# Performance work log

Measured on AMD Instinct MI355X. Metric: run time of the kernel, lower is better.

The kernel has to match this reference:

```python
import jax, jax.numpy as jnp
import numpy as np

EMB = 1024
HEADS = 16
HEAD_DIM = EMB // HEADS


def setup_inputs() -> dict:
    key = jax.random.key(0)
    ks = jax.random.split(key, 5)
    x = jax.random.normal(ks[0], (2, 2048, EMB), dtype=jnp.float32)
    # per-head projection params, stacked over heads: [H, E, D]
    Wq = jax.random.normal(ks[1], (HEADS, EMB, HEAD_DIM), dtype=jnp.float32)
    Wk = jax.random.normal(ks[2], (HEADS, EMB, HEAD_DIM), dtype=jnp.float32)
    Wv = jax.random.normal(ks[3], (HEADS, EMB, HEAD_DIM), dtype=jnp.float32)
    # output projection (torch Linear weight [out, in], bias=False)
    Wo = jax.random.normal(ks[4], (EMB, EMB), dtype=jnp.float32) * (1.0 / np.sqrt(EMB))
    return {"x": x, "Wq": Wq, "Wk": Wk, "Wv": Wv, "Wo": Wo}


def reference(x, Wq, Wk, Wv, Wo):
    B, T, E = x.shape
    # per-head projections: [B, H, T, D]
    q = jnp.einsum('bte,hed->bhtd', x, Wq)
    k = jnp.einsum('bte,hed->bhtd', x, Wk)
    v = jnp.einsum('bte,hed->bhtd', x, Wv)
    scale = 1.0 / jnp.sqrt(jnp.asarray(HEAD_DIM, dtype=x.dtype))
    scores = jnp.einsum('bhtd,bhsd->bhts', q, k) * scale  # [B,H,T,T]
    s = jax.nn.softmax(scores, axis=-1)
    out = jnp.einsum('bhts,bhsd->bhtd', s, v)
    # concat heads along last dim in head order: [B, T, H*D]
    combined = jnp.transpose(out, (0, 2, 1, 3)).reshape(B, T, E)
    # residual + output projection (Linear bias=False: y = combined @ Wo.T)
    return x + combined @ Wo.T
```

## Files before the change

### kernel.cpp

```cpp
#include <hip/hip_runtime.h>

#define EMB   1024
#define HEADS 16
#define HDIM  64
#define BATCH 2
#define SEQ   2048
#define MROWS (BATCH*SEQ)
#define STR   40

typedef __attribute__((ext_vector_type(8))) short bf16x8;
typedef __attribute__((ext_vector_type(4))) float f32x4;
typedef unsigned short u16;

__device__ __forceinline__ u16 f2bf(float f) {
    unsigned u = __float_as_uint(f);
    u += 0x7fffu + ((u >> 16) & 1u);
    return (u16)(u >> 16);
}
__device__ __forceinline__ float bf2f(u16 h) {
    return __uint_as_float((unsigned)h << 16);
}

__global__ __launch_bounds__(256)
void xsplit(const float* __restrict__ X, u16* __restrict__ Xh,
            u16* __restrict__ Xl)
{
    int i = (blockIdx.x * 256 + threadIdx.x) * 8;
#pragma unroll
    for (int half = 0; half < 2; ++half) {
        float4 v = *(const float4*)(X + i + half * 4);
        ushort4 hi, lo;
        hi.x = f2bf(v.x); lo.x = f2bf(v.x - bf2f(hi.x));
        hi.y = f2bf(v.y); lo.y = f2bf(v.y - bf2f(hi.y));
        hi.z = f2bf(v.z); lo.z = f2bf(v.z - bf2f(hi.z));
        hi.w = f2bf(v.w); lo.w = f2bf(v.w - bf2f(hi.w));
        *(ushort4*)(Xh + i + half * 4) = hi;
        *(ushort4*)(Xl + i + half * 4) = lo;
    }
}

__global__ __launch_bounds__(256)
void wtrans(const float* __restrict__ Wq, const float* __restrict__ Wk,
            u16* __restrict__ Qth, u16* __restrict__ Qtl,
            u16* __restrict__ Kth, u16* __restrict__ Ktl)
{
    const float* W  = blockIdx.z ? Wk  : Wq;
    u16* Oh         = blockIdx.z ? Kth : Qth;
    u16* Ol         = blockIdx.z ? Ktl : Qtl;
    const int h  = blockIdx.y;
    const int d  = threadIdx.x & 63;
    const int e0 = (blockIdx.x * 4 + (threadIdx.x >> 6)) * 8;

    const float* src = W + ((size_t)h * EMB + e0) * HDIM + d;
    ushort4 h0, h1, l0, l1;
    float v; u16 hv;
    v = src[0 * 64]; hv = f2bf(v); h0.x = hv; l0.x = f2bf(v - bf2f(hv));
    v = src[1 * 64]; hv = f2bf(v); h0.y = hv; l0.y = f2bf(v - bf2f(hv));
    v = src[2 * 64]; hv = f2bf(v); h0.z = hv; l0.z = f2bf(v - bf2f(hv));
    v = src[3 * 64]; hv = f2bf(v); h0.w = hv; l0.w = f2bf(v - bf2f(hv));
    v = src[4 * 64]; hv = f2bf(v); h1.x = hv; l1.x = f2bf(v - bf2f(hv));
    v = src[5 * 64]; hv = f2bf(v); h1.y = hv; l1.y = f2bf(v - bf2f(hv));
    v = src[6 * 64]; hv = f2bf(v); h1.z = hv; l1.z = f2bf(v - bf2f(hv));
    v = src[7 * 64]; hv = f2bf(v); h1.w = hv; l1.w = f2bf(v - bf2f(hv));

    size_t obase = ((size_t)h * HDIM + d) * EMB + e0;
    *(ushort4*)(Oh + obase)     = h0;
    *(ushort4*)(Oh + obase + 4) = h1;
    *(ushort4*)(Ol + obase)     = l0;
    *(ushort4*)(Ol + obase + 4) = l1;
}

__global__ __launch_bounds__(256)
void wtrans_v(const float* __restrict__ Wv, u16* __restrict__ Vth)
{
    const int h  = blockIdx.y;
    const int d  = threadIdx.x & 63;
    const int e0 = (blockIdx.x * 4 + (threadIdx.x >> 6)) * 8;
    const float* src = Wv + ((size_t)h * EMB + e0) * HDIM + d;
    ushort4 h0, h1;
    h0.x = f2bf(src[0 * 64]); h0.y = f2bf(src[1 * 64]);
    h0.z = f2bf(src[2 * 64]); h0.w = f2bf(src[3 * 64]);
    h1.x = f2bf(src[4 * 64]); h1.y = f2bf(src[5 * 64]);
    h1.z = f2bf(src[6 * 64]); h1.w = f2bf(src[7 * 64]);
    size_t obase = ((size_t)h * HDIM + d) * EMB + e0;
    *(ushort4*)(Vth + obase)     = h0;
    *(ushort4*)(Vth + obase + 4) = h1;
}

__global__ __launch_bounds__(256)
void conv_bf16(const float* __restrict__ src, u16* __restrict__ dst)
{
    int i = (blockIdx.x * 256 + threadIdx.x) * 4;
    float4 v = *(const float4*)(src + i);
    ushort4 o;
    o.x = f2bf(v.x); o.y = f2bf(v.y); o.z = f2bf(v.z); o.w = f2bf(v.w);
    *(ushort4*)(dst + i) = o;
}

__global__ __launch_bounds__(256)
void qkv_z01(const u16* __restrict__ Xh, const u16* __restrict__ Xl,
             const u16* __restrict__ Wqh, const u16* __restrict__ Wql,
             const u16* __restrict__ Wkh, const u16* __restrict__ Wkl,
             u16* __restrict__ Qh, u16* __restrict__ Ql,
             u16* __restrict__ Kh, u16* __restrict__ Kl)
{
    const int z  = blockIdx.z;
    const int m0 = blockIdx.x * 128;
    const int n0 = blockIdx.y * 128;
    const int t    = threadIdx.x;
    const int wave = t >> 6, lane = t & 63;
    const int wm = wave & 1, wn = wave >> 1;
    const int l16 = lane & 15, quad = lane >> 4;

    __shared__ u16 Ahs[128][STR];
    __shared__ u16 Als[128][STR];
    __shared__ u16 Bhs[128][STR];
    __shared__ u16 Bls[128][STR];

    const u16* Bh_g = z ? Wkh : Wqh;
    const u16* Bl_g = z ? Wkl : Wql;

    const int ar0 = t >> 2, ak = (t & 3) * 8, ar1 = ar0 + 64;

    f32x4 acc[4][4];
#pragma unroll
    for (int i = 0; i < 4; ++i)
#pragma unroll
        for (int j = 0; j < 4; ++j) acc[i][j] = (f32x4){0.f, 0.f, 0.f, 0.f};

    bf16x8 cur[8], nxt[8];
#define QK_LOAD(dst, kk)                                                        \
    do {                                                                        \
        dst[0] = *(const bf16x8*)(Xh  + (size_t)(m0 + ar0) * EMB + (kk) + ak);  \
        dst[1] = *(const bf16x8*)(Xh  + (size_t)(m0 + ar1) * EMB + (kk) + ak);  \
        dst[2] = *(const bf16x8*)(Xl  + (size_t)(m0 + ar0) * EMB + (kk) + ak);  \
        dst[3] = *(const bf16x8*)(Xl  + (size_t)(m0 + ar1) * EMB + (kk) + ak);  \
        dst[4] = *(const bf16x8*)(Bh_g + (size_t)(n0 + ar0) * EMB + (kk) + ak); \
        dst[5] = *(const bf16x8*)(Bh_g + (size_t)(n0 + ar1) * EMB + (kk) + ak); \
        dst[6] = *(const bf16x8*)(Bl_g + (size_t)(n0 + ar0) * EMB + (kk) + ak); \
        dst[7] = *(const bf16x8*)(Bl_g + (size_t)(n0 + ar1) * EMB + (kk) + ak); \
    } while (0)

    QK_LOAD(cur, 0);

    for (int k0 = 0; k0 < EMB; k0 += 32) {
        __syncthreads();
        *(bf16x8*)&Ahs[ar0][ak] = cur[0];  *(bf16x8*)&Ahs[ar1][ak] = cur[1];
        *(bf16x8*)&Als[ar0][ak] = cur[2];  *(bf16x8*)&Als[ar1][ak] = cur[3];
        *(bf16x8*)&Bhs[ar0][ak] = cur[4];  *(bf16x8*)&Bhs[ar1][ak] = cur[5];
        *(bf16x8*)&Bls[ar0][ak] = cur[6];  *(bf16x8*)&Bls[ar1][ak] = cur[7];
        __syncthreads();

        const int kn = (k0 + 32 < EMB) ? k0 + 32 : 0;
        QK_LOAD(nxt, kn);

        bf16x8 B4h[4], B4l[4];
#pragma unroll
        for (int j = 0; j < 4; ++j) {
            B4h[j] = *(const bf16x8*)&Bhs[wn * 64 + 16 * j + l16][quad * 8];
            B4l[j] = *(const bf16x8*)&Bls[wn * 64 + 16 * j + l16][quad * 8];
        }
#pragma unroll
        for (int i = 0; i < 4; ++i) {
            bf16x8 Ai_h = *(const bf16x8*)&Ahs[wm * 64 + 16 * i + l16][quad * 8];
            bf16x8 Ai_l = *(const bf16x8*)&Als[wm * 64 + 16 * i + l16][quad * 8];
#pragma unroll
            for (int j = 0; j < 4; ++j) {
                acc[i][j] = __builtin_amdgcn_mfma_f32_16x16x32_bf16(Ai_h, B4h[j], acc[i][j], 0, 0, 0);
                acc[i][j] = __builtin_amdgcn_mfma_f32_16x16x32_bf16(Ai_h, B4l[j], acc[i][j], 0, 0, 0);
                acc[i][j] = __builtin_amdgcn_mfma_f32_16x16x32_bf16(Ai_l, B4h[j], acc[i][j], 0, 0, 0);
            }
        }
#pragma unroll
        for (int q = 0; q < 8; ++q) cur[q] = nxt[q];
    }
#undef QK_LOAD

    const int b = m0 >> 11;
    const int h = (n0 + wn * 64) >> 6;
    u16* Oh = z ? Kh : Qh;
    u16* Ol = z ? Kl : Ql;
#pragma unroll
    for (int i = 0; i < 4; ++i)
#pragma unroll
        for (int r = 0; r < 4; ++r) {
            int tt = (m0 & (SEQ - 1)) + wm * 64 + 16 * i + quad * 4 + r;
            size_t rowbase = ((size_t)(b * HEADS + h) * SEQ + tt) * HDIM;
#pragma unroll
            for (int j = 0; j < 4; ++j) {
                int d = 16 * j + l16;
                float v = acc[i][j][r];
                u16 hv = f2bf(v);
                Oh[rowbase + d] = hv;
                Ol[rowbase + d] = f2bf(v - bf2f(hv));
            }
        }
}

__global__ __launch_bounds__(256)
void qkv_v(const u16* __restrict__ Xh, const u16* __restrict__ Wvt,
           u16* __restrict__ Vt)
{
    const int m0 = blockIdx.x * 128;
    const int n0 = blockIdx.y * 128;
    const int t    = threadIdx.x;
    const int wave = t >> 6, lane = t & 63;
    const int wm = wave & 1, wn = wave >> 1;
    const int l16 = lane & 15, quad = lane >> 4;

    __shared__ u16 Ahs[128][STR];
    __shared__ u16 Bhs[128][STR];

    const int ar0 = t >> 2, ak = (t & 3) * 8, ar1 = ar0 + 64;

    f32x4 acc[4][4];
#pragma unroll
    for (int i = 0; i < 4; ++i)
#pragma unroll
        for (int j = 0; j < 4; ++j) acc[i][j] = (f32x4){0.f, 0.f, 0.f, 0.f};

    bf16x8 cur[4], nxt[4];
#define V_LOAD(dst, kk)                                                         \
    do {                                                                        \
        dst[0] = *(const bf16x8*)(Xh  + (size_t)(m0 + ar0) * EMB + (kk) + ak);  \
        dst[1] = *(const bf16x8*)(Xh  + (size_t)(m0 + ar1) * EMB + (kk) + ak);  \
        dst[2] = *(const bf16x8*)(Wvt + (size_t)(n0 + ar0) * EMB + (kk) + ak);  \
        dst[3] = *(const bf16x8*)(Wvt + (size_t)(n0 + ar1) * EMB + (kk) + ak);  \
    } while (0)

    V_LOAD(cur, 0);

    for (int k0 = 0; k0 < EMB; k0 += 32) {
        __syncthreads();
        *(bf16x8*)&Ahs[ar0][ak] = cur[0];  *(bf16x8*)&Ahs[ar1][ak] = cur[1];
        *(bf16x8*)&Bhs[ar0][ak] = cur[2];  *(bf16x8*)&Bhs[ar1][ak] = cur[3];
        __syncthreads();

        const int kn = (k0 + 32 < EMB) ? k0 + 32 : 0;
        V_LOAD(nxt, kn);

        bf16x8 B4[4];
#pragma unroll
        for (int j = 0; j < 4; ++j)
            B4[j] = *(const bf16x8*)&Bhs[wn * 64 + 16 * j + l16][quad * 8];
#pragma unroll
        for (int i = 0; i < 4; ++i) {
            bf16x8 Ai = *(const bf16x8*)&Ahs[wm * 64 + 16 * i + l16][quad * 8];
#pragma unroll
            for (int j = 0; j < 4; ++j)
                acc[i][j] = __builtin_amdgcn_mfma_f32_16x16x32_bf16(Ai, B4[j], acc[i][j], 0, 0, 0);
        }
#pragma unroll
        for (int q = 0; q < 4; ++q) cur[q] = nxt[q];
    }
#undef V_LOAD

    const int b = m0 >> 11;
    const int h = (n0 + wn * 64) >> 6;
#pragma unroll
    for (int i = 0; i < 4; ++i)
#pragma unroll
        for (int j = 0; j < 4; ++j) {
            int d  = 16 * j + l16;
            int tt = (m0 & (SEQ - 1)) + wm * 64 + 16 * i + quad * 4;
            ushort4 o;
            o.x = f2bf(acc[i][j][0]); o.y = f2bf(acc[i][j][1]);
            o.z = f2bf(acc[i][j][2]); o.w = f2bf(acc[i][j][3]);
            *(ushort4*)(Vt + ((size_t)(b * HEADS + h) * HDIM + d) * SEQ + tt) = o;
        }
}

__global__ __launch_bounds__(256)
void attn_mfma(const u16* __restrict__ Qh, const u16* __restrict__ Ql,
               const u16* __restrict__ Kh, const u16* __restrict__ Kl,
               const u16* __restrict__ Vt, u16* __restrict__ Cb)
{
    const int qt0  = blockIdx.x * 64;
    const int bh   = blockIdx.y;
    const int t    = threadIdx.x;
    const int wave = t >> 6;
    const int lane = t & 63;
    const int l16  = lane & 15;
    const int quad = lane >> 4;

    __shared__ u16 Ksh[64][72];
    __shared__ u16 Ksl[64][72];
    __shared__ u16 Vs [64][72];
    __shared__ u16 Ps [64][72];

    const size_t bh_off = (size_t)bh * SEQ * HDIM;
    const u16* Qhb = Qh + bh_off;
    const u16* Qlb = Ql + bh_off;
    const u16* Khb = Kh + bh_off;
    const u16* Klb = Kl + bh_off;
    const u16* Vtb = Vt + bh_off;

    bf16x8 aQh[2], aQl[2];
    {
        const int qrow = qt0 + wave * 16 + l16;
        const u16* bH = Qhb + (size_t)qrow * HDIM + quad * 8;
        const u16* bL = Qlb + (size_t)qrow * HDIM + quad * 8;
        aQh[0] = *(const bf16x8*)(bH);
        aQh[1] = *(const bf16x8*)(bH + 32);
        aQl[0] = *(const bf16x8*)(bL);
        aQl[1] = *(const bf16x8*)(bL + 32);
    }

    f32x4 accO[4];
    float m_i = -1e30f, l_i = 0.f;
#pragma unroll
    for (int j = 0; j < 4; ++j) accO[j] = (f32x4){0.f, 0.f, 0.f, 0.f};

    const int r0 = t >> 3,          c0 = (t & 7) * 8;
    const int r1 = (t + 256) >> 3,  c1 = (t & 7) * 8;

    bf16x8 cur[6], nxt[6];
#define KV_LOAD(dst, ss)                                                       \
    do {                                                                       \
        dst[0] = *(const bf16x8*)(Khb + (size_t)((ss) + r0) * HDIM + c0);      \
        dst[1] = *(const bf16x8*)(Khb + (size_t)((ss) + r1) * HDIM + c1);      \
        dst[2] = *(const bf16x8*)(Klb + (size_t)((ss) + r0) * HDIM + c0);      \
        dst[3] = *(const bf16x8*)(Klb + (size_t)((ss) + r1) * HDIM + c1);      \
        dst[4] = *(const bf16x8*)(Vtb + (size_t)r0 * SEQ + (ss) + c0);         \
        dst[5] = *(const bf16x8*)(Vtb + (size_t)r1 * SEQ + (ss) + c1);         \
    } while (0)

    KV_LOAD(cur, 0);

    for (int s0 = 0; s0 < SEQ; s0 += 64) {
        __syncthreads();
        *(bf16x8*)&Ksh[r0][c0] = cur[0];  *(bf16x8*)&Ksh[r1][c1] = cur[1];
        *(bf16x8*)&Ksl[r0][c0] = cur[2];  *(bf16x8*)&Ksl[r1][c1] = cur[3];
        *(bf16x8*)&Vs [r0][c0] = cur[4];  *(bf16x8*)&Vs [r1][c1] = cur[5];
        __syncthreads();

        const int sn = (s0 + 64 < SEQ) ? s0 + 64 : 0;
        KV_LOAD(nxt, sn);

        f32x4 accS[4];
#pragma unroll
        for (int i = 0; i < 4; ++i) accS[i] = (f32x4){0.f, 0.f, 0.f, 0.f};
#pragma unroll
        for (int c = 0; c < 2; ++c) {
#pragma unroll
            for (int i = 0; i < 4; ++i) {
                bf16x8 kh_ = *(const bf16x8*)&Ksh[16 * i + l16][c * 32 + quad * 8];
                bf16x8 kl_ = *(const bf16x8*)&Ksl[16 * i + l16][c * 32 + quad * 8];
                accS[i] = __builtin_amdgcn_mfma_f32_16x16x32_bf16(kh_, aQh[c], accS[i], 0, 0, 0);
                accS[i] = __builtin_amdgcn_mfma_f32_16x16x32_bf16(kl_, aQh[c], accS[i], 0, 0, 0);
                accS[i] = __builtin_amdgcn_mfma_f32_16x16x32_bf16(kh_, aQl[c], accS[i], 0, 0, 0);
            }
        }
#pragma unroll
        for (int i = 0; i < 4; ++i) accS[i] *= 0.125f;

        float vmax = fmaxf(fmaxf(accS[0][0], accS[0][1]), fmaxf(accS[0][2], accS[0][3]));
#pragma unroll
        for (int i = 1; i < 4; ++i)
            vmax = fmaxf(vmax, fmaxf(fmaxf(accS[i][0], accS[i][1]),
                                     fmaxf(accS[i][2], accS[i][3])));
        vmax = fmaxf(vmax, __shfl_xor(vmax, 16, 64));
        vmax = fmaxf(vmax, __shfl_xor(vmax, 32, 64));
        float mn   = fmaxf(m_i, vmax);
        float alph = __expf(m_i - mn);
        m_i = mn;
        float P[4][4], s = 0.f;
#pragma unroll
        for (int i = 0; i < 4; ++i)
#pragma unroll
            for (int r = 0; r < 4; ++r) {
                P[i][r] = __expf(accS[i][r] - mn);
                s += P[i][r];
            }
        s += __shfl_xor(s, 16, 64);
        s += __shfl_xor(s, 32, 64);
        l_i = l_i * alph + s;
#pragma unroll
        for (int j = 0; j < 4; ++j) accO[j] *= alph;

#pragma unroll
        for (int i = 0; i < 4; ++i) {
            ushort4 o;
            o.x = f2bf(P[i][0]); o.y = f2bf(P[i][1]);
            o.z = f2bf(P[i][2]); o.w = f2bf(P[i][3]);
            *(ushort4*)&Ps[wave * 16 + l16][16 * i + quad * 4] = o;
        }

#pragma unroll
        for (int c = 0; c < 2; ++c) {
            bf16x8 bP = *(const bf16x8*)&Ps[wave * 16 + l16][c * 32 + quad * 8];
#pragma unroll
            for (int j = 0; j < 4; ++j) {
                bf16x8 aV = *(const bf16x8*)&Vs[16 * j + l16][c * 32 + quad * 8];
                accO[j] = __builtin_amdgcn_mfma_f32_16x16x32_bf16(aV, bP, accO[j], 0, 0, 0);
            }
        }
#pragma unroll
        for (int q = 0; q < 6; ++q) cur[q] = nxt[q];
    }
#undef KV_LOAD

    const int b = bh >> 4, h = bh & 15;
    const int row = qt0 + wave * 16 + l16;
    const float inv = 1.f / l_i;
#pragma unroll
    for (int j = 0; j < 4; ++j) {
        ushort4 o;
        o.x = f2bf(accO[j][0] * inv); o.y = f2bf(accO[j][1] * inv);
        o.z = f2bf(accO[j][2] * inv); o.w = f2bf(accO[j][3] * inv);
        *(ushort4*)&Cb[((size_t)b * SEQ + row) * EMB + h * HDIM + 16 * j + quad * 4] = o;
    }
}

__global__ __launch_bounds__(256)
void oproj_mfma(const u16* __restrict__ Cb, const u16* __restrict__ Woh,
                const float* __restrict__ X, float* __restrict__ Y)
{
    const int m0 = blockIdx.x * 128;
    const int n0 = blockIdx.y * 128;
    const int t    = threadIdx.x;
    const int wave = t >> 6, lane = t & 63;
    const int wm = wave & 1, wn = wave >> 1;
    const int l16 = lane & 15, quad = lane >> 4;

    __shared__ u16 Ahs[128][STR];
    __shared__ u16 Bhs[128][STR];

    const int ar0 = t >> 2, ak = (t & 3) * 8, ar1 = ar0 + 64;

    f32x4 acc[4][4];
#pragma unroll
    for (int i = 0; i < 4; ++i)
#pragma unroll
        for (int j = 0; j < 4; ++j) acc[i][j] = (f32x4){0.f, 0.f, 0.f, 0.f};

    bf16x8 cur[4], nxt[4];
#define O_LOAD(dst, kk)                                                         \
    do {                                                                        \
        dst[0] = *(const bf16x8*)(Cb  + (size_t)(m0 + ar0) * EMB + (kk) + ak);  \
        dst[1] = *(const bf16x8*)(Cb  + (size_t)(m0 + ar1) * EMB + (kk) + ak);  \
        dst[2] = *(const bf16x8*)(Woh + (size_t)(n0 + ar0) * EMB + (kk) + ak);  \
        dst[3] = *(const bf16x8*)(Woh + (size_t)(n0 + ar1) * EMB + (kk) + ak);  \
    } while (0)

    O_LOAD(cur, 0);

    for (int k0 = 0; k0 < EMB; k0 += 32) {
        __syncthreads();
        *(bf16x8*)&Ahs[ar0][ak] = cur[0];  *(bf16x8*)&Ahs[ar1][ak] = cur[1];
        *(bf16x8*)&Bhs[ar0][ak] = cur[2];  *(bf16x8*)&Bhs[ar1][ak] = cur[3];
        __syncthreads();

        const int kn = (k0 + 32 < EMB) ? k0 + 32 : 0;
        O_LOAD(nxt, kn);

        bf16x8 B4[4];
#pragma unroll
        for (int j = 0; j < 4; ++j)
            B4[j] = *(const bf16x8*)&Bhs[wn * 64 + 16 * j + l16][quad * 8];
#pragma unroll
        for (int i = 0; i < 4; ++i) {
            bf16x8 Ai = *(const bf16x8*)&Ahs[wm * 64 + 16 * i + l16][quad * 8];
#pragma unroll
            for (int j = 0; j < 4; ++j)
                acc[i][j] = __builtin_amdgcn_mfma_f32_16x16x32_bf16(Ai, B4[j], acc[i][j], 0, 0, 0);
        }
#pragma unroll
        for (int q = 0; q < 4; ++q) cur[q] = nxt[q];
    }
#undef O_LOAD

#pragma unroll
    for (int i = 0; i < 4; ++i)
#pragma unroll
        for (int r = 0; r < 4; ++r) {
            int m = m0 + wm * 64 + 16 * i + quad * 4 + r;
#pragma unroll
            for (int j = 0; j < 4; ++j) {
                int n = n0 + wn * 64 + 16 * j + l16;
                Y[(size_t)m * EMB + n] = acc[i][j][r] + X[(size_t)m * EMB + n];
            }
        }
}

extern "C" void kernel_launch(void* const* d_in, const int* in_sizes, int n_in,
                              void* d_out, int out_size, void* d_ws,
                              size_t ws_size, hipStream_t stream)
{
    const float* x  = (const float*)d_in[0];
    const float* Wq = (const float*)d_in[1];
    const float* Wk = (const float*)d_in[2];
    const float* Wv = (const float*)d_in[3];
    const float* Wo = (const float*)d_in[4];
    float* Y = (float*)d_out;

    const size_t NPER = (size_t)MROWS * EMB;
    u16* base  = (u16*)d_ws;
    u16* Qh    = base;
    u16* Ql    = Qh + NPER;
    u16* Kh    = Ql + NPER;
    u16* Kl    = Kh + NPER;
    u16* Vt    = Kl + NPER;
    u16* Xh    = Vt + NPER;
    u16* Xl    = Xh + NPER;
    u16* Wtq_h = Xl + NPER;
    u16* Wtq_l = Wtq_h + EMB * EMB;
    u16* Wtk_h = Wtq_l + EMB * EMB;
    u16* Wtk_l = Wtk_h + EMB * EMB;
    u16* Wvt   = Wtq_h;
    u16* Cb    = Xh;
    u16* Woh   = Xl;

    xsplit<<<dim3(NPER / 2048), 256, 0, stream>>>(x, Xh, Xl);
    wtrans<<<dim3(32, 16, 2), 256, 0, stream>>>(Wq, Wk, Wtq_h, Wtq_l,
                                                Wtk_h, Wtk_l);
    qkv_z01<<<dim3(32, 8, 2), 256, 0, stream>>>(Xh, Xl, Wtq_h, Wtq_l,
                                                Wtk_h, Wtk_l, Qh, Ql, Kh, Kl);
    wtrans_v<<<dim3(32, 16), 256, 0, stream>>>(Wv, Wvt);
    conv_bf16<<<dim3(EMB * EMB / 1024), 256, 0, stream>>>(Wo, Woh);
    qkv_v<<<dim3(32, 8), 256, 0, stream>>>(Xh, Wvt, Vt);
    attn_mfma<<<dim3(SEQ / 64, BATCH * HEADS), 256, 0, stream>>>(Qh, Ql, Kh, Kl,
                                                                 Vt, Cb);
    oproj_mfma<<<dim3(32, 8), 256, 0, stream>>>(Cb, Woh, x, Y);
}
```

Baseline: 297.9 us.

## Fuse prep kernels, fold softmax scale into Q, swizzle attention LDS, use exp2

Merges the four small conversion/transpose kernels into two launches to cut launch overhead. Q is pre-scaled by log2(e)/sqrt(D) in the projection epilogue so attention can drop its per-tile multiply and use the hardware exp2. Attention shared-memory tiles switch from padded rows to an XOR-swizzled layout to reduce bank conflicts. P is packed to bf16 by truncation via byte permute instead of round-to-nearest, which costs a little accuracy.

```diff
diff --git a/kernel.cpp b/kernel.cpp
--- a/kernel.cpp
+++ b/kernel.cpp
@@ -7,6 +7,7 @@
 #define SEQ   2048
 #define MROWS (BATCH*SEQ)
 #define STR   40
+#define QSCALE 0.1803368801111204f
 
 typedef __attribute__((ext_vector_type(8))) short bf16x8;
 typedef __attribute__((ext_vector_type(4))) float f32x4;
@@ -20,81 +21,96 @@
 __device__ __forceinline__ float bf2f(u16 h) {
     return __uint_as_float((unsigned)h << 16);
 }
+__device__ __forceinline__ float fast_exp2(float x) {
+#if __has_builtin(__builtin_amdgcn_exp2f)
+    return __builtin_amdgcn_exp2f(x);
+#else
+    return __expf(x * 0.6931471805599453f);
+#endif
+}
+__device__ __forceinline__ unsigned pk_trunc(float lo, float hi) {
+    return __builtin_amdgcn_perm(__float_as_uint(hi), __float_as_uint(lo),
+                                 0x07060302u);
+}
+
+#define SWZ(r, ch) ((((r) << 6)) + ((((ch) ^ ((r) & 7))) << 3))
 
 __global__ __launch_bounds__(256)
-void xsplit(const float* __restrict__ X, u16* __restrict__ Xh,
-            u16* __restrict__ Xl)
-{
-    int i = (blockIdx.x * 256 + threadIdx.x) * 8;
-#pragma unroll
-    for (int half = 0; half < 2; ++half) {
-        float4 v = *(const float4*)(X + i + half * 4);
-        ushort4 hi, lo;
-        hi.x = f2bf(v.x); lo.x = f2bf(v.x - bf2f(hi.x));
-        hi.y = f2bf(v.y); lo.y = f2bf(v.y - bf2f(hi.y));
-        hi.z = f2bf(v.z); lo.z = f2bf(v.z - bf2f(hi.z));
-        hi.w = f2bf(v.w); lo.w = f2bf(v.w - bf2f(hi.w));
-        *(ushort4*)(Xh + i + half * 4) = hi;
-        *(ushort4*)(Xl + i + half * 4) = lo;
+void prep1(const float* __restrict__ X, const float* __restrict__ Wq,
+           const float* __restrict__ Wk,
+           u16* __restrict__ Xh, u16* __restrict__ Xl,
+           u16* __restrict__ Qth, u16* __restrict__ Qtl,
+           u16* __restrict__ Kth, u16* __restrict__ Ktl)
+{
+    const int bx = blockIdx.x;
+    if (bx < 2048) {
+        int i = (bx * 256 + threadIdx.x) * 8;
+#pragma unroll
+        for (int half = 0; half < 2; ++half) {
+            float4 v = *(const float4*)(X + i + half * 4);
+            ushort4 hi, lo;
+            hi.x = f2bf(v.x); lo.x = f2bf(v.x - bf2f(hi.x));
+            hi.y = f2bf(v.y); lo.y = f2bf(v.y - bf2f(hi.y));
+            hi.z = f2bf(v.z); lo.z = f2bf(v.z - bf2f(hi.z));
+            hi.w = f2bf(v.w); lo.w = f2bf(v.w - bf2f(hi.w));
+            *(ushort4*)(Xh + i + half * 4) = hi;
+            *(ushort4*)(Xl + i + half * 4) = lo;
+        }
+    } else {
+        const int f = bx - 2048;
+        const int z = f >> 9, y = (f >> 5) & 15, x = f & 31;
+        const float* W  = z ? Wk  : Wq;
+        u16* Oh         = z ? Kth : Qth;
+        u16* Ol         = z ? Ktl : Qtl;
+        const int d  = threadIdx.x & 63;
+        const int e0 = (x * 4 + (threadIdx.x >> 6)) * 8;
+        const float* src = W + ((size_t)y * EMB + e0) * HDIM + d;
+        ushort4 h0, h1, l0, l1;
+        float v; u16 hv;
+        v = src[0 * 64]; hv = f2bf(v); h0.x = hv; l0.x = f2bf(v - bf2f(hv));
+        v = src[1 * 64]; hv = f2bf(v); h0.y = hv; l0.y = f2bf(v - bf2f(hv));
+        v = src[2 * 64]; hv = f2bf(v); h0.z = hv; l0.z = f2bf(v - bf2f(hv));
+        v = src[3 * 64]; hv = f2bf(v); h0.w = hv; l0.w = f2bf(v - bf2f(hv));
+        v = src[4 * 64]; hv = f2bf(v); h1.x = hv; l1.x = f2bf(v - bf2f(hv));
+        v = src[5 * 64]; hv = f2bf(v); h1.y = hv; l1.y = f2bf(v - bf2f(hv));
+        v = src[6 * 64]; hv = f2bf(v); h1.z = hv; l1.z = f2bf(v - bf2f(hv));
+        v = src[7 * 64]; hv = f2bf(v); h1.w = hv; l1.w = f2bf(v - bf2f(hv));
+        size_t obase = ((size_t)y * HDIM + d) * EMB + e0;
+        *(ushort4*)(Oh + obase)     = h0;
+        *(ushort4*)(Oh + obase + 4) = h1;
+        *(ushort4*)(Ol + obase)     = l0;
+        *(ushort4*)(Ol + obase + 4) = l1;
     }
 }
 
 __global__ __launch_bounds__(256)
-void wtrans(const float* __restrict__ Wq, const float* __restrict__ Wk,
-            u16* __restrict__ Qth, u16* __restrict__ Qtl,
-            u16* __restrict__ Kth, u16* __restrict__ Ktl)
-{
-    const float* W  = blockIdx.z ? Wk  : Wq;
-    u16* Oh         = blockIdx.z ? Kth : Qth;
-    u16* Ol         = blockIdx.z ? Ktl : Qtl;
-    const int h  = blockIdx.y;
-    const int d  = threadIdx.x & 63;
-    const int e0 = (blockIdx.x * 4 + (threadIdx.x >> 6)) * 8;
-
-    const float* src = W + ((size_t)h * EMB + e0) * HDIM + d;
-    ushort4 h0, h1, l0, l1;
-    float v; u16 hv;
-    v = src[0 * 64]; hv = f2bf(v); h0.x = hv; l0.x = f2bf(v - bf2f(hv));
-    v = src[1 * 64]; hv = f2bf(v); h0.y = hv; l0.y = f2bf(v - bf2f(hv));
-    v = src[2 * 64]; hv = f2bf(v); h0.z = hv; l0.z = f2bf(v - bf2f(hv));
-    v = src[3 * 64]; hv = f2bf(v); h0.w = hv; l0.w = f2bf(v - bf2f(hv));
-    v = src[4 * 64]; hv = f2bf(v); h1.x = hv; l1.x = f2bf(v - bf2f(hv));
-    v = src[5 * 64]; hv = f2bf(v); h1.y = hv; l1.y = f2bf(v - bf2f(hv));
-    v = src[6 * 64]; hv = f2bf(v); h1.z = hv; l1.z = f2bf(v - bf2f(hv));
-    v = src[7 * 64]; hv = f2bf(v); h1.w = hv; l1.w = f2bf(v - bf2f(hv));
-
-    size_t obase = ((size_t)h * HDIM + d) * EMB + e0;
-    *(ushort4*)(Oh + obase)     = h0;
-    *(ushort4*)(Oh + obase + 4) = h1;
-    *(ushort4*)(Ol + obase)     = l0;
-    *(ushort4*)(Ol + obase + 4) = l1;
-}
-
-__global__ __launch_bounds__(256)
-void wtrans_v(const float* __restrict__ Wv, u16* __restrict__ Vth)
-{
-    const int h  = blockIdx.y;
-    const int d  = threadIdx.x & 63;
-    const int e0 = (blockIdx.x * 4 + (threadIdx.x >> 6)) * 8;
-    const float* src = Wv + ((size_t)h * EMB + e0) * HDIM + d;
-    ushort4 h0, h1;
-    h0.x = f2bf(src[0 * 64]); h0.y = f2bf(src[1 * 64]);
-    h0.z = f2bf(src[2 * 64]); h0.w = f2bf(src[3 * 64]);
-    h1.x = f2bf(src[4 * 64]); h1.y = f2bf(src[5 * 64]);
-    h1.z = f2bf(src[6 * 64]); h1.w = f2bf(src[7 * 64]);
-    size_t obase = ((size_t)h * HDIM + d) * EMB + e0;
-    *(ushort4*)(Vth + obase)     = h0;
-    *(ushort4*)(Vth + obase + 4) = h1;
-}
-
-__global__ __launch_bounds__(256)
-void conv_bf16(const float* __restrict__ src, u16* __restrict__ dst)
-{
-    int i = (blockIdx.x * 256 + threadIdx.x) * 4;
-    float4 v = *(const float4*)(src + i);
-    ushort4 o;
-    o.x = f2bf(v.x); o.y = f2bf(v.y); o.z = f2bf(v.z); o.w = f2bf(v.w);
-    *(ushort4*)(dst + i) = o;
+void prep2(const float* __restrict__ Wv, const float* __restrict__ Wo,
+           u16* __restrict__ Vth, u16* __restrict__ Woh)
+{
+    const int f = blockIdx.x;
+    if (f < 512) {
+        const int y = f >> 5, x = f & 31;
+        const int d  = threadIdx.x & 63;
+        const int e0 = (x * 4 + (threadIdx.x >> 6)) * 8;
+        const float* src = Wv + ((size_t)y * EMB + e0) * HDIM + d;
+        ushort4 h0, h1;
+        h0.x = f2bf(src[0 * 64]); h0.y = f2bf(src[1 * 64]);
+        h0.z = f2bf(src[2 * 64]); h0.w = f2bf(src[3 * 64]);
+        h1.x = f2bf(src[4 * 64]); h1.y = f2bf(src[5 * 64]);
+        h1.z = f2bf(src[6 * 64]); h1.w = f2bf(src[7 * 64]);
+        size_t obase = ((size_t)y * HDIM + d) * EMB + e0;
+        *(ushort4*)(Vth + obase)     = h0;
+        *(ushort4*)(Vth + obase + 4) = h1;
+    } else {
+        int i = ((f - 512) * 256 + threadIdx.x) * 8;
+#pragma unroll
+        for (int half = 0; half < 2; ++half) {
+            float4 v = *(const float4*)(Wo + i + half * 4);
+            ushort4 o;
+            o.x = f2bf(v.x); o.y = f2bf(v.y); o.z = f2bf(v.z); o.w = f2bf(v.w);
+            *(ushort4*)(Woh + i + half * 4) = o;
+        }
+    }
 }
 
 __global__ __launch_bounds__(256)
@@ -180,6 +196,7 @@
     const int h = (n0 + wn * 64) >> 6;
     u16* Oh = z ? Kh : Qh;
     u16* Ol = z ? Kl : Ql;
+    const float esc = z ? 1.0f : QSCALE;
 #pragma unroll
     for (int i = 0; i < 4; ++i)
 #pragma unroll
@@ -189,7 +206,7 @@
 #pragma unroll
             for (int j = 0; j < 4; ++j) {
                 int d = 16 * j + l16;
-                float v = acc[i][j][r];
+                float v = acc[i][j][r] * esc;
                 u16 hv = f2bf(v);
                 Oh[rowbase + d] = hv;
                 Ol[rowbase + d] = f2bf(v - bf2f(hv));
@@ -283,10 +300,10 @@
     const int l16  = lane & 15;
     const int quad = lane >> 4;
 
-    __shared__ u16 Ksh[64][72];
-    __shared__ u16 Ksl[64][72];
-    __shared__ u16 Vs [64][72];
-    __shared__ u16 Ps [64][72];
+    __shared__ u16 Ksh[4096];
+    __shared__ u16 Ksl[4096];
+    __shared__ u16 Vs [4096];
+    __shared__ u16 Ps [4096];
 
     const size_t bh_off = (size_t)bh * SEQ * HDIM;
     const u16* Qhb = Qh + bh_off;
@@ -311,27 +328,28 @@
 #pragma unroll
     for (int j = 0; j < 4; ++j) accO[j] = (f32x4){0.f, 0.f, 0.f, 0.f};
 
-    const int r0 = t >> 3,          c0 = (t & 7) * 8;
-    const int r1 = (t + 256) >> 3,  c1 = (t & 7) * 8;
+    const int sr0 = t >> 3, sch = t & 7, sr1 = sr0 + 32;
+    const int gc  = sch * 8;
+    const int so0 = SWZ(sr0, sch), so1 = SWZ(sr1, sch);
 
     bf16x8 cur[6], nxt[6];
 #define KV_LOAD(dst, ss)                                                       \
     do {                                                                       \
-        dst[0] = *(const bf16x8*)(Khb + (size_t)((ss) + r0) * HDIM + c0);      \
-        dst[1] = *(const bf16x8*)(Khb + (size_t)((ss) + r1) * HDIM + c1);      \
-        dst[2] = *(const bf16x8*)(Klb + (size_t)((ss) + r0) * HDIM + c0);      \
-        dst[3] = *(const bf16x8*)(Klb + (size_t)((ss) + r1) * HDIM + c1);      \
-        dst[4] = *(const bf16x8*)(Vtb + (size_t)r0 * SEQ + (ss) + c0);         \
-        dst[5] = *(const bf16x8*)(Vtb + (size_t)r1 * SEQ + (ss) + c1);         \
+        dst[0] = *(const bf16x8*)(Khb + (size_t)((ss) + sr0) * HDIM + gc);     \
+        dst[1] = *(const bf16x8*)(Khb + (size_t)((ss) + sr1) * HDIM + gc);     \
+        dst[2] = *(const bf16x8*)(Klb + (size_t)((ss) + sr0) * HDIM + gc);     \
+        dst[3] = *(const bf16x8*)(Klb + (size_t)((ss) + sr1) * HDIM + gc);     \
+        dst[4] = *(const bf16x8*)(Vtb + (size_t)sr0 * SEQ + (ss) + gc);        \
+        dst[5] = *(const bf16x8*)(Vtb + (size_t)sr1 * SEQ + (ss) + gc);        \
     } while (0)
 
     KV_LOAD(cur, 0);
 
     for (int s0 = 0; s0 < SEQ; s0 += 64) {
         __syncthreads();
-        *(bf16x8*)&Ksh[r0][c0] = cur[0];  *(bf16x8*)&Ksh[r1][c1] = cur[1];
-        *(bf16x8*)&Ksl[r0][c0] = cur[2];  *(bf16x8*)&Ksl[r1][c1] = cur[3];
-        *(bf16x8*)&Vs [r0][c0] = cur[4];  *(bf16x8*)&Vs [r1][c1] = cur[5];
+        *(bf16x8*)&Ksh[so0] = cur[0];  *(bf16x8*)&Ksh[so1] = cur[1];
+        *(bf16x8*)&Ksl[so0] = cur[2];  *(bf16x8*)&Ksl[so1] = cur[3];
+        *(bf16x8*)&Vs [so0] = cur[4];  *(bf16x8*)&Vs [so1] = cur[5];
         __syncthreads();
 
         const int sn = (s0 + 64 < SEQ) ? s0 + 64 : 0;
@@ -344,15 +362,13 @@
         for (int c = 0; c < 2; ++c) {
 #pragma unroll
             for (int i = 0; i < 4; ++i) {
-                bf16x8 kh_ = *(const bf16x8*)&Ksh[16 * i + l16][c * 32 + quad * 8];
-                bf16x8 kl_ = *(const bf16x8*)&Ksl[16 * i + l16][c * 32 + quad * 8];
+                bf16x8 kh_ = *(const bf16x8*)&Ksh[SWZ(16 * i + l16, 4 * c + quad)];
+                bf16x8 kl_ = *(const bf16x8*)&Ksl[SWZ(16 * i + l16, 4 * c + quad)];
                 accS[i] = __builtin_amdgcn_mfma_f32_16x16x32_bf16(kh_, aQh[c], accS[i], 0, 0, 0);
                 accS[i] = __builtin_amdgcn_mfma_f32_16x16x32_bf16(kl_, aQh[c], accS[i], 0, 0, 0);
                 accS[i] = __builtin_amdgcn_mfma_f32_16x16x32_bf16(kh_, aQl[c], accS[i], 0, 0, 0);
             }
         }
-#pragma unroll
-        for (int i = 0; i < 4; ++i) accS[i] *= 0.125f;
 
         float vmax = fmaxf(fmaxf(accS[0][0], accS[0][1]), fmaxf(accS[0][2], accS[0][3]));
 #pragma unroll
@@ -362,14 +378,14 @@
         vmax = fmaxf(vmax, __shfl_xor(vmax, 16, 64));
         vmax = fmaxf(vmax, __shfl_xor(vmax, 32, 64));
         float mn   = fmaxf(m_i, vmax);
-        float alph = __expf(m_i - mn);
+        float alph = fast_exp2(m_i - mn);
         m_i = mn;
         float P[4][4], s = 0.f;
 #pragma unroll
         for (int i = 0; i < 4; ++i)
 #pragma unroll
             for (int r = 0; r < 4; ++r) {
-                P[i][r] = __expf(accS[i][r] - mn);
+                P[i][r] = fast_exp2(accS[i][r] - mn);
                 s += P[i][r];
             }
         s += __shfl_xor(s, 16, 64);
@@ -378,20 +394,21 @@
 #pragma unroll
         for (int j = 0; j < 4; ++j) accO[j] *= alph;
 
+        const int prow = wave * 16 + l16;
 #pragma unroll
         for (int i = 0; i < 4; ++i) {
-            ushort4 o;
-            o.x = f2bf(P[i][0]); o.y = f2bf(P[i][1]);
-            o.z = f2bf(P[i][2]); o.w = f2bf(P[i][3]);
-            *(ushort4*)&Ps[wave * 16 + l16][16 * i + quad * 4] = o;
+            uint2 pv;
+            pv.x = pk_trunc(P[i][0], P[i][1]);
+            pv.y = pk_trunc(P[i][2], P[i][3]);
+            *(uint2*)&Ps[SWZ(prow, 2 * i + (quad >> 1)) + ((quad & 1) << 2)] = pv;
         }
 
 #pragma unroll
         for (int c = 0; c < 2; ++c) {
-            bf16x8 bP = *(const bf16x8*)&Ps[wave * 16 + l16][c * 32 + quad * 8];
+            bf16x8 bP = *(const bf16x8*)&Ps[SWZ(prow, 4 * c + quad)];
 #pragma unroll
             for (int j = 0; j < 4; ++j) {
-                bf16x8 aV = *(const bf16x8*)&Vs[16 * j + l16][c * 32 + quad * 8];
+                bf16x8 aV = *(const bf16x8*)&Vs[SWZ(16 * j + l16, 4 * c + quad)];
                 accO[j] = __builtin_amdgcn_mfma_f32_16x16x32_bf16(aV, bP, accO[j], 0, 0, 0);
             }
         }
@@ -511,13 +528,11 @@
     u16* Cb    = Xh;
     u16* Woh   = Xl;
 
-    xsplit<<<dim3(NPER / 2048), 256, 0, stream>>>(x, Xh, Xl);
-    wtrans<<<dim3(32, 16, 2), 256, 0, stream>>>(Wq, Wk, Wtq_h, Wtq_l,
-                                                Wtk_h, Wtk_l);
+    prep1<<<dim3(3072), 256, 0, stream>>>(x, Wq, Wk, Xh, Xl,
+                                          Wtq_h, Wtq_l, Wtk_h, Wtk_l);
     qkv_z01<<<dim3(32, 8, 2), 256, 0, stream>>>(Xh, Xl, Wtq_h, Wtq_l,
                                                 Wtk_h, Wtk_l, Qh, Ql, Kh, Kl);
-    wtrans_v<<<dim3(32, 16), 256, 0, stream>>>(Wv, Wvt);
-    conv_bf16<<<dim3(EMB * EMB / 1024), 256, 0, stream>>>(Wo, Woh);
+    prep2<<<dim3(1024), 256, 0, stream>>>(Wv, Wo, Wvt, Woh);
     qkv_v<<<dim3(32, 8), 256, 0, stream>>>(Xh, Wvt, Vt);
     attn_mfma<<<dim3(SEQ / 64, BATCH * HEADS), 256, 0, stream>>>(Qh, Ql, Kh, Kl,
                                                                  Vt, Cb);
```

After: 287.1 us. 1.04x faster.
